# Kernel optimization log

Hardware: AMD Instinct MI355X
Metric: run time of the kernel (lower is better)

## Reference

```python
import jax, jax.numpy as jnp
import numpy as np

D_MODEL = 2048
NUM_HEADS = 32
NUM_KV_HEADS = 8
HEAD_DIM = D_MODEL // NUM_HEADS  # 64
B, S = 2, 2048


def rotary_cos_sin(seq_len, head_dim, dtype=jnp.float32):
    inv_freq = 1.0 / (10000.0 ** (jnp.arange(0, head_dim, 2, dtype=jnp.float32) / head_dim))
    t = jnp.arange(seq_len, dtype=jnp.float32)
    freqs = t[:, None] * inv_freq[None, :]          # [S, hd/2]
    emb = jnp.concatenate([freqs, freqs], axis=-1)  # [S, hd]
    return emb.astype(dtype).reshape(1, seq_len, 1, head_dim), None  # placeholder


def apply_rotary_emb(x, cos, sin):
    # faithful to source: interleaved rotate-half, concatenated cos/sin
    x1 = x[..., ::2]
    x2 = x[..., 1::2]
    rotated = jnp.stack([-x2, x1], axis=-1).reshape(x.shape)
    return x * cos + rotated * sin


def setup_inputs() -> dict:
    key = jax.random.key(0)
    ks = jax.random.split(key, 5)
    sc = 0.02
    x = jax.random.normal(ks[0], (B, S, D_MODEL), dtype=jnp.float32)
    Wq = jax.random.normal(ks[1], (D_MODEL, D_MODEL), dtype=jnp.float32) * sc
    Wk = jax.random.normal(ks[2], (D_MODEL, NUM_KV_HEADS * HEAD_DIM), dtype=jnp.float32) * sc
    Wv = jax.random.normal(ks[3], (D_MODEL, NUM_KV_HEADS * HEAD_DIM), dtype=jnp.float32) * sc
    Wo = jax.random.normal(ks[4], (D_MODEL, D_MODEL), dtype=jnp.float32) * sc
    mask = jnp.tril(jnp.ones((S, S), dtype=jnp.int32))[None, None]  # [1,1,S,S] causal
    return {"x": x, "mask": mask, "Wq": Wq, "Wk": Wk, "Wv": Wv, "Wo": Wo}


def reference(x, mask, Wq, Wk, Wv, Wo):
    b, s, _ = x.shape
    q = (x @ Wq).reshape(b, s, NUM_HEADS, HEAD_DIM)
    k = (x @ Wk).reshape(b, s, NUM_KV_HEADS, HEAD_DIM)
    v = (x @ Wv).reshape(b, s, NUM_KV_HEADS, HEAD_DIM)

    inv_freq = 1.0 / (10000.0 ** (jnp.arange(0, HEAD_DIM, 2, dtype=jnp.float32) / HEAD_DIM))
    t = jnp.arange(s, dtype=jnp.float32)
    freqs = t[:, None] * inv_freq[None, :]
    emb = jnp.concatenate([freqs, freqs], axis=-1)         # [S, hd]
    cos = jnp.cos(emb)[None, :, None, :].astype(x.dtype)   # [1,S,1,hd]
    sin = jnp.sin(emb)[None, :, None, :].astype(x.dtype)

    q = apply_rotary_emb(q, cos, sin)
    k = apply_rotary_emb(k, cos, sin)

    rep = NUM_HEADS // NUM_KV_HEADS
    k = jnp.repeat(k, rep, axis=2)  # [B,S,H,hd]
    v = jnp.repeat(v, rep, axis=2)

    q = q.transpose(0, 2, 1, 3)  # [B,H,S,hd]
    k = k.transpose(0, 2, 1, 3)
    v = v.transpose(0, 2, 1, 3)

    scale = 1.0 / jnp.sqrt(jnp.asarray(HEAD_DIM, dtype=x.dtype))
    scores = jnp.einsum('bhqd,bhkd->bhqk', q, k) * scale
    scores = jnp.where(mask == 0, jnp.asarray(-jnp.inf, scores.dtype), scores)
    attn = jax.nn.softmax(scores, axis=-1)
    out = jnp.einsum('bhqk,bhkd->bhqd', attn, v)
    out = out.transpose(0, 2, 1, 3).reshape(b, s, D_MODEL)
    return out @ Wo
```

## Files before the change

### kernel.cpp

```cpp
#include <hip/hip_runtime.h>
#include <hip/hip_bf16.h>

typedef __bf16 bf16;
typedef __bf16 bf16x8 __attribute__((ext_vector_type(8)));
typedef float  f32x4  __attribute__((ext_vector_type(4)));

#define B_  2
#define S_  2048
#define H_  32
#define HK_ 8
#define D_  64
#define DM_ 2048
#define LDQ 3072

__device__ __forceinline__ void async_copy16(const bf16* g, bf16* l) {
    __builtin_amdgcn_global_load_lds((const __attribute__((address_space(1))) void*)g,
                                     (__attribute__((address_space(3))) void*)l,
                                     16, 0, 0);
}

__device__ __forceinline__ void tile_transpose(const float* __restrict__ in,
                                               bf16* __restrict__ out,
                                               int R, int C, int bx, int by,
                                               bf16 (*tile)[33], int tx, int ty) {
#pragma unroll
    for (int k = 0; k < 4; ++k)
        tile[ty + 8 * k][tx] = (bf16)in[(long)(by * 32 + ty + 8 * k) * C + bx * 32 + tx];
    __syncthreads();
#pragma unroll
    for (int k = 0; k < 4; ++k)
        out[(long)(bx * 32 + ty + 8 * k) * R + by * 32 + tx] = tile[tx][ty + 8 * k];
}

__global__ __launch_bounds__(256) void prep(const float* __restrict__ x,
                                            bf16* __restrict__ xb,
                                            const float* __restrict__ Wq,
                                            const float* __restrict__ Wk,
                                            const float* __restrict__ Wv,
                                            bf16* __restrict__ wT3) {
    __shared__ bf16 tile[32][33];
    const int tid = threadIdx.x;
    int bid = blockIdx.x;
    if (bid < 8192) {
        const long i = (long)bid * 256 + tid;
        const float4 v = ((const float4*)x)[i];
        union { bf16 h[4]; short4 s; } u;
        u.h[0] = (bf16)v.x; u.h[1] = (bf16)v.y; u.h[2] = (bf16)v.z; u.h[3] = (bf16)v.w;
        ((short4*)xb)[i] = u.s;
        return;
    }
    bid -= 8192;
    const int tx = tid & 31, ty = tid >> 5;
    if (bid < 4096)
        tile_transpose(Wq, wT3, 2048, 2048, bid & 63, bid >> 6, tile, tx, ty);
    else if (bid < 5120)
        tile_transpose(Wk, wT3 + 2048L * 2048, 2048, 512, (bid - 4096) & 15, (bid - 4096) >> 4, tile, tx, ty);
    else
        tile_transpose(Wv, wT3 + 2560L * 2048, 2048, 512, (bid - 5120) & 15, (bid - 5120) >> 4, tile, tx, ty);
}

__global__ __launch_bounds__(256) void postgemm(bf16* __restrict__ qkv,
                                                bf16* __restrict__ vT,
                                                const float* __restrict__ Wo,
                                                bf16* __restrict__ wT3) {
    __shared__ bf16 tile[32][33];
    const int tid = threadIdx.x;
    int bid = blockIdx.x;
    if (bid < 20480) {
        const int idx = bid * 256 + tid;
        const int i  = idx & 31;
        const int s  = (idx >> 5) & (S_ - 1);
        const int ord = idx >> 16;
        const int b  = (ord >= 40) ? 1 : 0;
        const int hh = ord - 40 * b;
        const int colOff = (hh < 32) ? hh * 64 : 2048 + (hh - 32) * 64;
        const long base = (long)(b * S_ + s) * LDQ + colOff;
        const float x0 = (float)qkv[base + 2 * i];
        const float x1 = (float)qkv[base + 2 * i + 1];
        const float t = (float)s;
        const float c10k = 9.210340371976184f;
        const int i0 = (2 * i) & 31;
        const int i1 = (2 * i + 1) & 31;
        const float f0 = t * expf(-(float)i0 * (c10k / 32.f));
        const float f1 = t * expf(-(float)i1 * (c10k / 32.f));
        const float o0 = x0 * cosf(f0) - x1 * sinf(f0);
        const float o1 = x1 * cosf(f1) + x0 * sinf(f1);
        qkv[base + 2 * i]     = (bf16)o0;
        qkv[base + 2 * i + 1] = (bf16)o1;
        return;
    }
    bid -= 20480;
    const int tx = tid & 31, ty = tid >> 5;
    if (bid < 2048) {
        const int sx = bid & 63, dy = (bid >> 6) & 1, p = bid >> 7;
        const int b = p >> 3, h = p & 7;
        const int s0 = sx * 32, d0 = dy * 32;
        const bf16* ip = qkv + (long)(b * S_) * LDQ + 2560 + h * 64;
#pragma unroll
        for (int k = 0; k < 4; ++k)
            tile[ty + 8 * k][tx] = ip[(long)(s0 + ty + 8 * k) * LDQ + d0 + tx];
        __syncthreads();
        bf16* op = vT + ((long)(b * HK_ + h) * D_) * S_;
#pragma unroll
        for (int k = 0; k < 4; ++k)
            op[(long)(d0 + ty + 8 * k) * S_ + s0 + tx] = tile[tx][ty + 8 * k];
        return;
    }
    bid -= 2048;
    tile_transpose(Wo, wT3, 2048, 2048, bid & 63, bid >> 6, tile, tx, ty);
}

template <typename OutT>
__global__ __launch_bounds__(256, 3) void gemm_tb(const bf16* __restrict__ A, int lda,
                                                  const bf16* __restrict__ Bt, int ldb,
                                                  OutT* __restrict__ C, int ldc, int K) {
    constexpr int ABUF = 128 * 32;
    constexpr int BUF  = 2 * ABUF;
    __shared__ __align__(16) bf16 lds[3 * BUF];

    const int tid  = threadIdx.x;
    const int w    = tid >> 6;
    const int lane = tid & 63;
    const int quad = lane >> 4;
    const int l16  = lane & 15;
    const int wr   = w >> 1;
    const int wc   = w & 1;
    const long m0  = (long)blockIdx.y * 128;
    const long n0  = (long)blockIdx.x * 128;

    const int srow = lane >> 2;
    const int schk = ((lane & 3) ^ ((lane >> 3) & 3)) * 8;
    const bf16* Ag = A  + (m0 + w * 32 + srow) * lda + schk;
    const bf16* Bg = Bt + (n0 + w * 32 + srow) * ldb + schk;

    const int rchk = (quad ^ ((l16 >> 1) & 3)) * 8;
    const int aoff = (wr * 64 + l16) * 32 + rchk;
    const int boff = (wc * 64 + l16) * 32 + rchk;

#define STAGE(buf, k0)                                                          \
    do {                                                                        \
        async_copy16(Ag + (k0),            (buf) + (w * 32) * 32);              \
        async_copy16(Ag + 16 * lda + (k0), (buf) + (w * 32 + 16) * 32);         \
        async_copy16(Bg + (k0),            (buf) + ABUF + (w * 32) * 32);       \
        async_copy16(Bg + 16 * ldb + (k0), (buf) + ABUF + (w * 32 + 16) * 32);  \
    } while (0)

    bf16* p0 = lds;
    bf16* p1 = lds + BUF;
    bf16* p2 = lds + 2 * BUF;

    STAGE(p0, 0);
    STAGE(p1, 32);

    f32x4 acc[4][4] = {};
    const int nt = K / 32;

    for (int t = 0; t < nt; ++t) {
        if (t < nt - 1) { asm volatile("s_waitcnt vmcnt(4)" ::: "memory"); }
        else            { asm volatile("s_waitcnt vmcnt(0)" ::: "memory"); }
        __builtin_amdgcn_s_barrier();
        __builtin_amdgcn_sched_barrier(0);
        if (t + 2 < nt) STAGE(p2, (t + 2) * 32);
        bf16x8 a[4], b[4];
#pragma unroll
        for (int m = 0; m < 4; ++m) a[m] = *(const bf16x8*)(p0 + aoff + m * 16 * 32);
#pragma unroll
        for (int n = 0; n < 4; ++n) b[n] = *(const bf16x8*)(p0 + ABUF + boff + n * 16 * 32);
        asm volatile("s_waitcnt lgkmcnt(0)" ::: "memory");
        __builtin_amdgcn_sched_barrier(0);
        __builtin_amdgcn_s_setprio(1);
#pragma unroll
        for (int m = 0; m < 4; ++m)
#pragma unroll
            for (int n = 0; n < 4; ++n)
                acc[m][n] = __builtin_amdgcn_mfma_f32_16x16x32_bf16(a[m], b[n], acc[m][n], 0, 0, 0);
        __builtin_amdgcn_s_setprio(0);
        bf16* tp = p0; p0 = p1; p1 = p2; p2 = tp;
    }
#undef STAGE

#pragma unroll
    for (int m = 0; m < 4; ++m) {
        const long r = m0 + wr * 64 + m * 16 + quad * 4;
#pragma unroll
        for (int n = 0; n < 4; ++n) {
            const long c = n0 + wc * 64 + n * 16 + l16;
#pragma unroll
            for (int reg = 0; reg < 4; ++reg)
                C[(r + reg) * ldc + c] = (OutT)acc[m][n][reg];
        }
    }
}

__global__ __launch_bounds__(256, 4) void attn_fused(bf16* qkv,
                                                     const bf16* __restrict__ Vt) {
    __shared__ __align__(16) bf16 Ks[64 * 64];
    __shared__ __align__(16) bf16 Vs[64 * 64];
    __shared__ __align__(16) bf16 Pbuf[4][32 * 72];
    const int tid  = threadIdx.x;
    const int w    = tid >> 6;
    const int lane = tid & 63;
    const int quad = lane >> 4;
    const int l16  = lane & 15;
    const int r8   = lane >> 3;
    const int sw   = (lane & 7) ^ r8;
    const int x7   = l16 & 7;

    const int bid = blockIdx.x;
    const int grp = bid & 15;
    const int qi  = 63 - (bid >> 4);
    const int hk  = grp & 7;
    const int b   = grp >> 3;
    const int h   = hk * 4 + w;

    const bf16* kp = qkv + (long)(b * S_) * LDQ + 2048 + hk * 64;
    const bf16* vp = Vt + (long)(b * HK_ + hk) * D_ * S_;
    bf16* P = &Pbuf[w][0];

    const float C1 = 0.18033688011112043f;
    const float C2 = 23.083120654223415f;
    const f32x4 zero = {0.f, 0.f, 0.f, 0.f};

    const int q0 = qi * 32;
    bf16* qp = qkv + (long)(b * S_ + q0) * LDQ + h * 64;

    bf16x8 aq[2][2];
#pragma unroll
    for (int i = 0; i < 2; ++i)
#pragma unroll
        for (int half = 0; half < 2; ++half)
            aq[i][half] = *(const bf16x8*)(qp + (long)(i * 16 + l16) * LDQ + half * 32 + quad * 8);

    f32x4 accO[2][4] = {};
    float ps[2][4] = {};

    const int nkt = q0 / 64 + 1;
    for (int kt = 0; kt < nkt; ++kt) {
        const int kb = kt * 64;
        __syncthreads();
#pragma unroll
        for (int t = 0; t < 2; ++t) {
            const int rloc = w * 16 + t * 8;
            async_copy16(kp + (long)(kb + rloc + r8) * LDQ + sw * 8, Ks + rloc * 64);
            async_copy16(vp + (long)(rloc + r8) * S_ + kb + sw * 8,  Vs + rloc * 64);
        }
        __syncthreads();

        const bool lastTile = (kt == nkt - 1);
#pragma unroll
        for (int g = 0; g < 4; ++g) {
            const int krow = g * 16 + l16;
            const bf16x8 bk0 = *(const bf16x8*)(Ks + krow * 64 + ((quad ^ x7) * 8));
            const bf16x8 bk1 = *(const bf16x8*)(Ks + krow * 64 + (((quad + 4) ^ x7) * 8));
#pragma unroll
            for (int i = 0; i < 2; ++i) {
                __builtin_amdgcn_s_setprio(1);
                f32x4 t = __builtin_amdgcn_mfma_f32_16x16x32_bf16(aq[i][0], bk0, zero, 0, 0, 0);
                f32x4 s = __builtin_amdgcn_mfma_f32_16x16x32_bf16(aq[i][1], bk1, t, 0, 0, 0);
                __builtin_amdgcn_s_setprio(0);
#pragma unroll
                for (int rg = 0; rg < 4; ++rg) {
                    float e;
                    if (lastTile) {
                        const int key  = kb + g * 16 + l16;
                        const int qrow = q0 + i * 16 + quad * 4 + rg;
                        e = (key <= qrow)
                          ? __builtin_amdgcn_exp2f(fminf(s[rg] * C1 - C2, 10.f)) : 0.f;
                    } else {
                        e = __builtin_amdgcn_exp2f(fminf(s[rg] * C1 - C2, 10.f));
                    }
                    ps[i][rg] += e;
                    P[(i * 16 + quad * 4 + rg) * 72 + g * 16 + l16] = (bf16)e;
                }
            }
        }
        __asm__ volatile("s_waitcnt lgkmcnt(0)" ::: "memory");
#pragma unroll
        for (int i = 0; i < 2; ++i) {
            const bf16x8 aP0 = *(const bf16x8*)(P + (i * 16 + l16) * 72 + quad * 8);
            const bf16x8 aP1 = *(const bf16x8*)(P + (i * 16 + l16) * 72 + 32 + quad * 8);
#pragma unroll
            for (int c = 0; c < 4; ++c) {
                const int vrow = c * 16 + l16;
                const bf16x8 bv0 = *(const bf16x8*)(Vs + vrow * 64 + ((quad ^ x7) * 8));
                const bf16x8 bv1 = *(const bf16x8*)(Vs + vrow * 64 + (((quad + 4) ^ x7) * 8));
                __builtin_amdgcn_s_setprio(1);
                accO[i][c] = __builtin_amdgcn_mfma_f32_16x16x32_bf16(aP0, bv0, accO[i][c], 0, 0, 0);
                accO[i][c] = __builtin_amdgcn_mfma_f32_16x16x32_bf16(aP1, bv1, accO[i][c], 0, 0, 0);
                __builtin_amdgcn_s_setprio(0);
            }
        }
        __asm__ volatile("s_waitcnt lgkmcnt(0)" ::: "memory");
    }

#pragma unroll
    for (int off = 1; off < 16; off <<= 1)
#pragma unroll
        for (int i = 0; i < 2; ++i)
#pragma unroll
            for (int rg = 0; rg < 4; ++rg)
                ps[i][rg] += __shfl_xor(ps[i][rg], off, 64);
    float invl[2][4];
#pragma unroll
    for (int i = 0; i < 2; ++i)
#pragma unroll
        for (int rg = 0; rg < 4; ++rg) invl[i][rg] = 1.f / ps[i][rg];

#pragma unroll
    for (int i = 0; i < 2; ++i)
#pragma unroll
        for (int c = 0; c < 4; ++c)
#pragma unroll
            for (int rg = 0; rg < 4; ++rg) {
                const long row = (long)(b * S_ + q0 + i * 16 + quad * 4 + rg);
                qkv[row * LDQ + h * 64 + c * 16 + l16] = (bf16)(accO[i][c][rg] * invl[i][rg]);
            }
}

extern "C" void kernel_launch(void* const* d_in, const int* in_sizes, int n_in,
                              void* d_out, int out_size, void* d_ws, size_t ws_size,
                              hipStream_t stream) {
    (void)in_sizes; (void)n_in; (void)out_size; (void)ws_size;
    const float* x  = (const float*)d_in[0];
    const float* Wq = (const float*)d_in[2];
    const float* Wk = (const float*)d_in[3];
    const float* Wv = (const float*)d_in[4];
    const float* Wo = (const float*)d_in[5];
    float* out = (float*)d_out;

    bf16* qkv = (bf16*)d_ws;
    bf16* wT3 = qkv + 4096L * 3072;
    bf16* xb  = (bf16*)d_out;
    bf16* vT  = xb + 4096L * 2048;

    const dim3 blk(256);

    prep<<<dim3(14336), blk, 0, stream>>>(x, xb, Wq, Wk, Wv, wT3);

    gemm_tb<bf16><<<dim3(24, 32), blk, 0, stream>>>(
        xb, 2048, wT3, 2048, qkv, LDQ, 2048);

    postgemm<<<dim3(26624), blk, 0, stream>>>(qkv, vT, Wo, wT3);

    attn_fused<<<dim3(B_ * HK_ * 64), blk, 0, stream>>>(qkv, vT);

    gemm_tb<float><<<dim3(16, 32), blk, 0, stream>>>(
        qkv, LDQ, wT3, 2048, out, 2048, 2048);
}
```

Before: 308.0 us.

## Double attention block to 512 threads covering 64 query rows per K/V tile

The attention kernel now uses 512-thread blocks with 8 waves, each block handling 64 query rows (two 32-row halves per head) instead of 32. Every K/V tile loaded into LDS is therefore shared by twice as many waves, halving global K/V traffic and the number of blocks. The grid shrinks to 512 blocks, which lowers occupancy flexibility and makes causal load imbalance coarser. Separately, the RoPE pass loads and stores bf16 pairs as a single 32-bit access instead of two scalar ones.

```diff
diff --git a/kernel.cpp b/kernel.cpp
--- a/kernel.cpp
+++ b/kernel.cpp
@@ -75,8 +75,9 @@
         const int hh = ord - 40 * b;
         const int colOff = (hh < 32) ? hh * 64 : 2048 + (hh - 32) * 64;
         const long base = (long)(b * S_ + s) * LDQ + colOff;
-        const float x0 = (float)qkv[base + 2 * i];
-        const float x1 = (float)qkv[base + 2 * i + 1];
+        const ushort2 u = *(const ushort2*)(qkv + base + 2 * i);
+        const float x0 = (float)*(const bf16*)&u.x;
+        const float x1 = (float)*(const bf16*)&u.y;
         const float t = (float)s;
         const float c10k = 9.210340371976184f;
         const int i0 = (2 * i) & 31;
@@ -85,8 +86,10 @@
         const float f1 = t * expf(-(float)i1 * (c10k / 32.f));
         const float o0 = x0 * cosf(f0) - x1 * sinf(f0);
         const float o1 = x1 * cosf(f1) + x0 * sinf(f1);
-        qkv[base + 2 * i]     = (bf16)o0;
-        qkv[base + 2 * i + 1] = (bf16)o1;
+        ushort2 o;
+        *(bf16*)&o.x = (bf16)o0;
+        *(bf16*)&o.y = (bf16)o1;
+        *(ushort2*)(qkv + base + 2 * i) = o;
         return;
     }
     bid -= 20480;
@@ -192,11 +195,11 @@
     }
 }
 
-__global__ __launch_bounds__(256, 4) void attn_fused(bf16* qkv,
+__global__ __launch_bounds__(512, 4) void attn_fused(bf16* qkv,
                                                      const bf16* __restrict__ Vt) {
     __shared__ __align__(16) bf16 Ks[64 * 64];
     __shared__ __align__(16) bf16 Vs[64 * 64];
-    __shared__ __align__(16) bf16 Pbuf[4][32 * 72];
+    __shared__ __align__(16) bf16 Pbuf[8][32 * 72];
     const int tid  = threadIdx.x;
     const int w    = tid >> 6;
     const int lane = tid & 63;
@@ -208,10 +211,11 @@
 
     const int bid = blockIdx.x;
     const int grp = bid & 15;
-    const int qi  = 63 - (bid >> 4);
+    const int qi  = 31 - (bid >> 4);
     const int hk  = grp & 7;
     const int b   = grp >> 3;
-    const int h   = hk * 4 + w;
+    const int h   = hk * 4 + (w & 3);
+    const int ro  = (w >> 2) * 32;
 
     const bf16* kp = qkv + (long)(b * S_) * LDQ + 2048 + hk * 64;
     const bf16* vp = Vt + (long)(b * HK_ + hk) * D_ * S_;
@@ -221,8 +225,8 @@
     const float C2 = 23.083120654223415f;
     const f32x4 zero = {0.f, 0.f, 0.f, 0.f};
 
-    const int q0 = qi * 32;
-    bf16* qp = qkv + (long)(b * S_ + q0) * LDQ + h * 64;
+    const int q0 = qi * 64;
+    bf16* qp = qkv + (long)(b * S_ + q0 + ro) * LDQ + h * 64;
 
     bf16x8 aq[2][2];
 #pragma unroll
@@ -234,16 +238,12 @@
     f32x4 accO[2][4] = {};
     float ps[2][4] = {};
 
-    const int nkt = q0 / 64 + 1;
+    const int nkt = qi + 1;
     for (int kt = 0; kt < nkt; ++kt) {
         const int kb = kt * 64;
         __syncthreads();
-#pragma unroll
-        for (int t = 0; t < 2; ++t) {
-            const int rloc = w * 16 + t * 8;
-            async_copy16(kp + (long)(kb + rloc + r8) * LDQ + sw * 8, Ks + rloc * 64);
-            async_copy16(vp + (long)(rloc + r8) * S_ + kb + sw * 8,  Vs + rloc * 64);
-        }
+        async_copy16(kp + (long)(kb + w * 8 + r8) * LDQ + sw * 8, Ks + (w * 8) * 64);
+        async_copy16(vp + (long)(w * 8 + r8) * S_ + kb + sw * 8,  Vs + (w * 8) * 64);
         __syncthreads();
 
         const bool lastTile = (kt == nkt - 1);
@@ -263,7 +263,7 @@
                     float e;
                     if (lastTile) {
                         const int key  = kb + g * 16 + l16;
-                        const int qrow = q0 + i * 16 + quad * 4 + rg;
+                        const int qrow = q0 + ro + i * 16 + quad * 4 + rg;
                         e = (key <= qrow)
                           ? __builtin_amdgcn_exp2f(fminf(s[rg] * C1 - C2, 10.f)) : 0.f;
                     } else {
@@ -312,7 +312,7 @@
         for (int c = 0; c < 4; ++c)
 #pragma unroll
             for (int rg = 0; rg < 4; ++rg) {
-                const long row = (long)(b * S_ + q0 + i * 16 + quad * 4 + rg);
+                const long row = (long)(b * S_ + q0 + ro + i * 16 + quad * 4 + rg);
                 qkv[row * LDQ + h * 64 + c * 16 + l16] = (bf16)(accO[i][c][rg] * invl[i][rg]);
             }
 }
@@ -342,7 +342,7 @@
 
     postgemm<<<dim3(26624), blk, 0, stream>>>(qkv, vT, Wo, wT3);
 
-    attn_fused<<<dim3(B_ * HK_ * 64), blk, 0, stream>>>(qkv, vT);
+    attn_fused<<<dim3(512), dim3(512), 0, stream>>>(qkv, vT);
 
     gemm_tb<float><<<dim3(16, 32), blk, 0, stream>>>(
         qkv, LDQ, wT3, 2048, out, 2048, 2048);
```

New measurement: 313.7 us. About the same (+1.9%).
